# Kernel tuning notes

Measured on AMD Instinct MI355X. Metric: run time of the kernel, lower is better.

The kernel has to match this reference:

```python
import jax, jax.numpy as jnp
import numpy as np
import math

D = 512; NA = 128; NC = 256; NB = 128; BATCH = 4; H = 8
EA, EC, EB = 4, 6, 4
KA, KC, KB = 2, 1, 2
F = 4 * D  # expert_ff_mult * embed_dim
N_TOTAL = NA + NC + NB


def setup_inputs() -> dict:
    key = jax.random.key(0)
    ks = jax.random.split(key, 16)
    s = 0.02
    def nrm(k, shape, scale=s):
        return jax.random.normal(k, shape, dtype=jnp.float32) * scale
    return {
        'tokens_A': jax.random.normal(ks[0], (BATCH, NA, D), dtype=jnp.float32),
        'tokens_B': jax.random.normal(ks[1], (BATCH, NB, D), dtype=jnp.float32),
        'tokens_C': jax.random.normal(ks[2], (BATCH, NC, D), dtype=jnp.float32),
        'ln1_g': jnp.ones((3, D), jnp.float32), 'ln1_b': jnp.zeros((3, D), jnp.float32),
        'ln2_g': jnp.ones((3, D), jnp.float32), 'ln2_b': jnp.zeros((3, D), jnp.float32),
        'Wqkv': nrm(ks[3], (3 * D, D)), 'bqkv': jnp.zeros((3 * D,), jnp.float32),
        'Wo': nrm(ks[4], (D, D)), 'bo': jnp.zeros((D,), jnp.float32),
        'Wr_A': nrm(ks[5], (D, EA)), 'br_A': jnp.zeros((EA,), jnp.float32),
        'W1_A': nrm(ks[6], (EA, D, F)), 'b1_A': jnp.zeros((EA, F), jnp.float32),
        'W2_A': nrm(ks[7], (EA, F, D)), 'b2_A': jnp.zeros((EA, D), jnp.float32),
        'Wr_C': nrm(ks[8], (D, EC)), 'br_C': jnp.zeros((EC,), jnp.float32),
        'W1_C': nrm(ks[9], (EC, D, F)), 'b1_C': jnp.zeros((EC, F), jnp.float32),
        'W2_C': nrm(ks[10], (EC, F, D)), 'b2_C': jnp.zeros((EC, D), jnp.float32),
        'Wr_B': nrm(ks[11], (D, EB)), 'br_B': jnp.zeros((EB,), jnp.float32),
        'W1_B': nrm(ks[12], (EB, D, F)), 'b1_B': jnp.zeros((EB, F), jnp.float32),
        'W2_B': nrm(ks[13], (EB, F, D)), 'b2_B': jnp.zeros((EB, D), jnp.float32),
    }


def _ln(x, g, b, eps=1e-5):
    m = jnp.mean(x, axis=-1, keepdims=True)
    v = jnp.var(x, axis=-1, keepdims=True)
    return (x - m) * jax.lax.rsqrt(v + eps) * g + b


def _directed_mask_bias():
    # segments: 0=A, 1=C, 2=B in [A|C|B] order; query may attend upstream groups only
    seg = jnp.concatenate([jnp.zeros(NA), jnp.ones(NC), 2.0 * jnp.ones(NB)])
    allowed = seg[None, :] <= seg[:, None]  # (N, N)
    return jnp.where(allowed, 0.0, -1e9).astype(jnp.float32)


def _mha(x, Wqkv, bqkv, Wo, bo, mask_bias):
    B, N, _ = x.shape
    qkv = x @ Wqkv.T + bqkv  # (B, N, 3D)
    q, k, v = jnp.split(qkv, 3, axis=-1)
    hd = D // H
    def heads(t):
        return t.reshape(B, N, H, hd).transpose(0, 2, 1, 3)  # (B, H, N, hd)
    q, k, v = heads(q), heads(k), heads(v)
    scores = jnp.einsum('bhqd,bhkd->bhqk', q, k) / math.sqrt(hd) + mask_bias[None, None]
    attn = jax.nn.softmax(scores, axis=-1)
    o = jnp.einsum('bhqk,bhkd->bhqd', attn, v).transpose(0, 2, 1, 3).reshape(B, N, D)
    return o @ Wo.T + bo


def _moe(x, Wr, br, W1, b1, W2, b2, k):
    # top-k routed expert FFN: softmax gates -> top-k renormalized -> dense combine
    probs = jax.nn.softmax(x @ Wr + br, axis=-1)  # (B, N, E)
    vals, idx = jax.lax.top_k(probs, k)
    vals = vals / jnp.sum(vals, axis=-1, keepdims=True)
    E = Wr.shape[1]
    gate = jnp.sum(jax.nn.one_hot(idx, E, dtype=x.dtype) * vals[..., None], axis=-2)  # (B, N, E)
    h = jax.nn.gelu(jnp.einsum('bnd,edf->benf', x, W1) + b1[None, :, None, :])
    y = jnp.einsum('benf,efd->bend', h, W2) + b2[None, :, None, :]
    return jnp.einsum('bne,bend->bnd', gate, y)


def reference(tokens_A, tokens_B, tokens_C, ln1_g, ln1_b, ln2_g, ln2_b,
              Wqkv, bqkv, Wo, bo,
              Wr_A, br_A, W1_A, b1_A, W2_A, b2_A,
              Wr_C, br_C, W1_C, b1_C, W2_C, b2_C,
              Wr_B, br_B, W1_B, b1_B, W2_B, b2_B):
    # 1-2. group-local pre-attention LN, concat [A | C | B]
    x = jnp.concatenate([
        _ln(tokens_A, ln1_g[0], ln1_b[0]),
        _ln(tokens_C, ln1_g[1], ln1_b[1]),
        _ln(tokens_B, ln1_g[2], ln1_b[2]),
    ], axis=1)
    # 3-4. shared directed self-attention + per-group residual
    attn = _mha(x, Wqkv, bqkv, Wo, bo, _directed_mask_bias())
    tA = tokens_A + attn[:, :NA]
    tC = tokens_C + attn[:, NA:NA + NC]
    tB = tokens_B + attn[:, NA + NC:]
    # 5. group-local pre-expert LN
    nA = _ln(tA, ln2_g[0], ln2_b[0])
    nC = _ln(tC, ln2_g[1], ln2_b[1])
    nB = _ln(tB, ln2_g[2], ln2_b[2])
    # 6-9. route A and C first, then B; residual add per group
    tA = tA + _moe(nA, Wr_A, br_A, W1_A, b1_A, W2_A, b2_A, KA)
    tC = tC + _moe(nC, Wr_C, br_C, W1_C, b1_C, W2_C, b2_C, KC)
    tB = tB + _moe(nB, Wr_B, br_B, W1_B, b1_B, W2_B, b2_B, KB)
    return jnp.concatenate([tA, tC, tB], axis=1)  # (B, NA+NC+NB, D)
```

## Files before the change

### kernel.cpp

```cpp
#include <hip/hip_runtime.h>
#include <hip/hip_bf16.h>
#include <cstdint>

#define DEV __device__ __forceinline__

using f32x4  = __attribute__((ext_vector_type(4))) float;
using bf16x8 = __attribute__((ext_vector_type(8))) __bf16;

static constexpr int D_    = 512;
static constexpr int ROWS  = 2048;
static constexpr int F_    = 2048;
static constexpr int NEXP  = 14;
static constexpr int NENT  = 3072;

#if defined(__has_builtin)
#if __has_builtin(__builtin_amdgcn_global_load_lds)
#define HAS_GLL 1
#endif
#endif

DEV unsigned short f2bf(float f) {
  unsigned int u = __builtin_bit_cast(unsigned int, f);
  unsigned int r = u + 0x7FFFu + ((u >> 16) & 1u);
  return (unsigned short)(r >> 16);
}
DEV unsigned int pack2(float a, float b) {
  return (unsigned int)f2bf(a) | ((unsigned int)f2bf(b) << 16);
}
DEV float gelu_tanh(float x) {
  float x3 = x * x * x;
  return 0.5f * x * (1.0f + tanhf(0.7978845608028654f * (x + 0.044715f * x3)));
}
DEV int prefix_base(const int* cnt, int e) {
  int base = 0;
  for (int i = 0; i < e; ++i) base += cnt[i];
  return base;
}

struct Shared128 { unsigned short As[128][72]; unsigned short Bs[64][72]; };

DEV void gemm128(const unsigned short* arow, const float* B, int ldb, int bcol0, int K,
                 f32x4 (&acc)[2][4], Shared128& sh)
{
  const int tid = threadIdx.x;
  const int lane = tid & 63, w = tid >> 6;
  const int ai = tid >> 1, ah = tid & 1;
  const int bj = tid >> 2, bq = tid & 3;
  for (int k0 = 0; k0 < K; k0 += 64) {
    __syncthreads();
    {
      const uint4* src = reinterpret_cast<const uint4*>(arow + k0 + ah * 32);
      uint4 v0 = src[0], v1 = src[1], v2 = src[2], v3 = src[3];
      uint4* dst = reinterpret_cast<uint4*>(&sh.As[ai][ah * 32]);
      dst[0] = v0; dst[1] = v1; dst[2] = v2; dst[3] = v3;
    }
    {
      const float4* src = reinterpret_cast<const float4*>(B + (size_t)(bcol0 + bj) * ldb + k0 + bq * 16);
      unsigned int pk[8];
      #pragma unroll
      for (int u = 0; u < 4; ++u) {
        float4 f = src[u];
        pk[u * 2]     = pack2(f.x, f.y);
        pk[u * 2 + 1] = pack2(f.z, f.w);
      }
      uint4* dst = reinterpret_cast<uint4*>(&sh.Bs[bj][bq * 16]);
      dst[0] = make_uint4(pk[0], pk[1], pk[2], pk[3]);
      dst[1] = make_uint4(pk[4], pk[5], pk[6], pk[7]);
    }
    __syncthreads();
    #pragma unroll
    for (int ks = 0; ks < 2; ++ks) {
      bf16x8 a[2], b[4];
      #pragma unroll
      for (int mi = 0; mi < 2; ++mi)
        a[mi] = *reinterpret_cast<const bf16x8*>(&sh.As[w * 32 + mi * 16 + (lane & 15)][ks * 32 + (lane >> 4) * 8]);
      #pragma unroll
      for (int ni = 0; ni < 4; ++ni)
        b[ni] = *reinterpret_cast<const bf16x8*>(&sh.Bs[ni * 16 + (lane & 15)][ks * 32 + (lane >> 4) * 8]);
      #pragma unroll
      for (int mi = 0; mi < 2; ++mi)
        #pragma unroll
        for (int ni = 0; ni < 4; ++ni)
          acc[mi][ni] = __builtin_amdgcn_mfma_f32_16x16x32_bf16(a[mi], b[ni], acc[mi][ni], 0, 0, 0);
    }
  }
}

struct __align__(16) SharedMoE { unsigned short As[64][72]; unsigned short Bs[8192]; };

DEV void gemm64x128L(const unsigned short* arow, const unsigned short* Bt,
                     f32x4 (&acc)[8], SharedMoE& sh)
{
  const int tid = threadIdx.x;
  const int lane = tid & 63, w = tid >> 6;
  const int ar = tid >> 2, aq = tid & 3;
  #pragma unroll
  for (int kt = 0; kt < 8; ++kt) {
    __syncthreads();
#ifdef HAS_GLL
    {
      const unsigned short* src = Bt + kt * 8192 + w * 2048 + lane * 8;
      unsigned short* dstBase = &sh.Bs[w * 2048];
      #pragma unroll
      for (int i = 0; i < 4; ++i)
        __builtin_amdgcn_global_load_lds(
            (const __attribute__((address_space(1))) unsigned int*)(src + i * 512),
            (__attribute__((address_space(3))) unsigned int*)(dstBase + i * 512),
            16, 0, 0);
    }
#else
    {
      const uint4* srcB = reinterpret_cast<const uint4*>(Bt + kt * 8192 + tid * 32);
      uint4 b0 = srcB[0], b1 = srcB[1], b2 = srcB[2], b3 = srcB[3];
      uint4* dstB = reinterpret_cast<uint4*>(&sh.Bs[tid * 32]);
      dstB[0] = b0; dstB[1] = b1; dstB[2] = b2; dstB[3] = b3;
    }
#endif
    {
      const uint4* srcA = reinterpret_cast<const uint4*>(arow + kt * 64 + aq * 16);
      uint4 a0 = srcA[0], a1 = srcA[1];
      uint4* dstA = reinterpret_cast<uint4*>(&sh.As[ar][aq * 16]);
      dstA[0] = a0; dstA[1] = a1;
    }
    __syncthreads();
    bf16x8 a0 = *reinterpret_cast<const bf16x8*>(&sh.As[w * 16 + (lane & 15)][0 * 32 + (lane >> 4) * 8]);
    bf16x8 a1 = *reinterpret_cast<const bf16x8*>(&sh.As[w * 16 + (lane & 15)][1 * 32 + (lane >> 4) * 8]);
    #pragma unroll
    for (int ni = 0; ni < 8; ++ni) {
      bf16x8 b0 = *reinterpret_cast<const bf16x8*>(&sh.Bs[(ni * 2 + 0) * 512 + lane * 8]);
      bf16x8 b1 = *reinterpret_cast<const bf16x8*>(&sh.Bs[(ni * 2 + 1) * 512 + lane * 8]);
      acc[ni] = __builtin_amdgcn_mfma_f32_16x16x32_bf16(a0, b0, acc[ni], 0, 0, 0);
      acc[ni] = __builtin_amdgcn_mfma_f32_16x16x32_bf16(a1, b1, acc[ni], 0, 0, 0);
    }
  }
}

__global__ __launch_bounds__(256) void k_ln(
    const float* tA, const float* tC, const float* tB,
    const float* g3, const float* b3, unsigned short* out)
{
  int r = blockIdx.x;
  int b = r >> 9, n = r & 511;
  int grp = n < 128 ? 0 : (n < 384 ? 1 : 2);
  const float* src = grp == 0 ? tA + (size_t)(b * 128 + n) * D_
                   : grp == 1 ? tC + (size_t)(b * 256 + n - 128) * D_
                              : tB + (size_t)(b * 128 + n - 384) * D_;
  int tid = threadIdx.x, lane = tid & 63, w = tid >> 6;
  float2 v = *reinterpret_cast<const float2*>(src + tid * 2);
  float s = v.x + v.y;
  float ss = v.x * v.x + v.y * v.y;
  #pragma unroll
  for (int off = 1; off < 64; off <<= 1) { s += __shfl_xor(s, off); ss += __shfl_xor(ss, off); }
  __shared__ float red[8];
  if (lane == 0) { red[w] = s; red[4 + w] = ss; }
  __syncthreads();
  float S  = red[0] + red[1] + red[2] + red[3];
  float SS = red[4] + red[5] + red[6] + red[7];
  float mean = S * (1.0f / 512.0f);
  float var  = SS * (1.0f / 512.0f) - mean * mean;
  float inv  = rsqrtf(var + 1e-5f);
  const float* gam = g3 + grp * D_;
  const float* bet = b3 + grp * D_;
  int d0 = tid * 2;
  out[(size_t)r * D_ + d0]     = f2bf((v.x - mean) * inv * gam[d0]     + bet[d0]);
  out[(size_t)r * D_ + d0 + 1] = f2bf((v.y - mean) * inv * gam[d0 + 1] + bet[d0 + 1]);
}

__global__ __launch_bounds__(256) void k_qkv_pack(
    const unsigned short* x, const float* Wqkv, const float* bqkv,
    unsigned short* Qg, unsigned short* Kg, unsigned short* Vg,
    const float* w1A, const float* w1C, const float* w1B,
    const float* w2A, const float* w2C, const float* w2B,
    unsigned short* W1P, unsigned short* W2P)
{
  __shared__ __align__(16) char smem[sizeof(Shared128)];
  int bid = blockIdx.x;
  int tid = threadIdx.x;
  if (bid < 384) {
    Shared128& sh = *reinterpret_cast<Shared128*>(smem);
    int bn = bid % 24, bm = (bid / 24) % 4, batch = bid / 96;
    int lane = tid & 63, w = tid >> 6;
    const unsigned short* arow = x + (size_t)(batch * 512 + bm * 128 + (tid >> 1)) * D_;
    f32x4 acc[2][4] = {};
    gemm128(arow, Wqkv, 512, bn * 64, 512, acc, sh);
    #pragma unroll
    for (int mi = 0; mi < 2; ++mi)
    #pragma unroll
    for (int ni = 0; ni < 4; ++ni)
    #pragma unroll
    for (int j = 0; j < 4; ++j) {
      int n = bm * 128 + w * 32 + mi * 16 + ((lane >> 4) << 2) + j;
      int col = bn * 64 + ni * 16 + (lane & 15);
      float val = acc[mi][ni][j] + bqkv[col];
      int part = col >> 9;
      int o = col & 511, h = o >> 6, d = o & 63;
      unsigned short* dst = part == 0 ? Qg : (part == 1 ? Kg : Vg);
      dst[(size_t)((batch * 8 + h) * 512 + n) * 64 + d] = f2bf(val);
    }
  } else {
    int pbid = bid - 384;
    int bx = pbid & 127, z = pbid >> 7;
    const float* src;
    unsigned short* dstbase;
    int ld, ntile, ktile, KT;
    if (z < 14) {
      int e = z;
      src = e < 4 ? w1A + (size_t)e * D_ * F_ : e < 10 ? w1C + (size_t)(e - 4) * D_ * F_ : w1B + (size_t)(e - 10) * D_ * F_;
      dstbase = W1P + (size_t)e * F_ * D_;
      ld = F_; KT = 8;
      ntile = bx >> 3; ktile = bx & 7;
    } else {
      int e = z - 14;
      src = e < 4 ? w2A + (size_t)e * F_ * D_ : e < 10 ? w2C + (size_t)(e - 4) * F_ * D_ : w2B + (size_t)(e - 10) * F_ * D_;
      dstbase = W2P + (size_t)e * D_ * F_;
      ld = D_; KT = 32;
      ntile = bx >> 5; ktile = bx & 31;
    }
    int k0 = ktile * 64, n0 = ntile * 128;
    auto sh = reinterpret_cast<unsigned short (*)[138]>(smem);
    {
      int r = tid >> 2, q = tid & 3;
      const float4* sp = reinterpret_cast<const float4*>(src + (size_t)(k0 + r) * ld + n0 + q * 32);
      unsigned int* shw = reinterpret_cast<unsigned int*>(&sh[r][q * 32]);
      #pragma unroll
      for (int u = 0; u < 8; ++u) {
        float4 v = sp[u];
        shw[u * 2]     = pack2(v.x, v.y);
        shw[u * 2 + 1] = pack2(v.z, v.w);
      }
    }
    __syncthreads();
    size_t tbase = (size_t)(ntile * KT + ktile) * 8192;
    #pragma unroll
    for (int i = 0; i < 4; ++i) {
      int p = tid + 256 * i;
      int f = p >> 6, l = p & 63;
      int ks = f & 1, ni = f >> 1;
      int nl = ni * 16 + (l & 15);
      int kl = ks * 32 + (l >> 4) * 8;
      unsigned short tmp[8];
      #pragma unroll
      for (int j = 0; j < 8; ++j) tmp[j] = sh[kl + j][nl];
      *reinterpret_cast<uint4*>(dstbase + tbase + (size_t)p * 8) = *reinterpret_cast<const uint4*>(tmp);
    }
  }
}

__global__ __launch_bounds__(64) void k_attn(const unsigned short* Qg, const unsigned short* Kg,
                                             const unsigned short* Vg, unsigned short* attn)
{
  __shared__ unsigned short Qs[16][72], Ks[64][72], VT[64][72], Ps[16][72];
  int qt16 = blockIdx.x, h = blockIdx.y, b = blockIdx.z;
  int lane = threadIdx.x;
  const unsigned short* Qb  = Qg + (size_t)((b * 8 + h) * 512) * 64;
  const unsigned short* Kbp = Kg + (size_t)((b * 8 + h) * 512) * 64;
  const unsigned short* Vbp = Vg + (size_t)((b * 8 + h) * 512) * 64;
  int q0 = qt16 * 16;
  {
    int row = lane >> 2, q4 = lane & 3;
    const uint4* src = reinterpret_cast<const uint4*>(Qb + (size_t)(q0 + row) * 64 + q4 * 16);
    uint4* dst = reinterpret_cast<uint4*>(&Qs[row][q4 * 16]);
    dst[0] = src[0]; dst[1] = src[1];
  }
  int nkt = qt16 < 8 ? 2 : (qt16 < 24 ? 6 : 8);
  float mrun[4] = { -1e30f, -1e30f, -1e30f, -1e30f };
  float lrun[4] = {};
  f32x4 o[4] = {};
  for (int kt = 0; kt < nkt; ++kt) {
    #pragma unroll
    for (int it = 0; it < 4; ++it) {
      int row = it * 16 + (lane >> 2), q4 = lane & 3;
      const uint4* ksrc = reinterpret_cast<const uint4*>(Kbp + (size_t)(kt * 64 + row) * 64 + q4 * 16);
      uint4* kdst = reinterpret_cast<uint4*>(&Ks[row][q4 * 16]);
      kdst[0] = ksrc[0]; kdst[1] = ksrc[1];
      union { uint4 u; unsigned short s[8]; } vv0, vv1;
      const uint4* vsrc = reinterpret_cast<const uint4*>(Vbp + (size_t)(kt * 64 + row) * 64 + q4 * 16);
      vv0.u = vsrc[0]; vv1.u = vsrc[1];
      #pragma unroll
      for (int jj = 0; jj < 8; ++jj) {
        VT[q4 * 16 + jj][row]     = vv0.s[jj];
        VT[q4 * 16 + 8 + jj][row] = vv1.s[jj];
      }
    }
    f32x4 s[4] = {};
    #pragma unroll
    for (int ks = 0; ks < 2; ++ks) {
      bf16x8 aq = *reinterpret_cast<const bf16x8*>(&Qs[lane & 15][ks * 32 + (lane >> 4) * 8]);
      #pragma unroll
      for (int cc = 0; cc < 4; ++cc) {
        bf16x8 bk = *reinterpret_cast<const bf16x8*>(&Ks[cc * 16 + (lane & 15)][ks * 32 + (lane >> 4) * 8]);
        s[cc] = __builtin_amdgcn_mfma_f32_16x16x32_bf16(aq, bk, s[cc], 0, 0, 0);
      }
    }
    #pragma unroll
    for (int rr = 0; rr < 4; ++rr) {
      float s0 = s[0][rr] * 0.125f, s1 = s[1][rr] * 0.125f;
      float s2 = s[2][rr] * 0.125f, s3 = s[3][rr] * 0.125f;
      float mx = fmaxf(fmaxf(s0, s1), fmaxf(s2, s3));
      #pragma unroll
      for (int off = 1; off < 16; off <<= 1) mx = fmaxf(mx, __shfl_xor(mx, off));
      float mn = fmaxf(mrun[rr], mx);
      float al = expf(mrun[rr] - mn);
      mrun[rr] = mn;
      float p0 = expf(s0 - mn), p1 = expf(s1 - mn), p2 = expf(s2 - mn), p3 = expf(s3 - mn);
      float ps = p0 + p1 + p2 + p3;
      #pragma unroll
      for (int off = 1; off < 16; off <<= 1) ps += __shfl_xor(ps, off);
      lrun[rr] = lrun[rr] * al + ps;
      #pragma unroll
      for (int n4 = 0; n4 < 4; ++n4) o[n4][rr] *= al;
      int prow = ((lane >> 4) << 2) + rr;
      Ps[prow][0 * 16 + (lane & 15)] = f2bf(p0);
      Ps[prow][1 * 16 + (lane & 15)] = f2bf(p1);
      Ps[prow][2 * 16 + (lane & 15)] = f2bf(p2);
      Ps[prow][3 * 16 + (lane & 15)] = f2bf(p3);
    }
    #pragma unroll
    for (int ks = 0; ks < 2; ++ks) {
      bf16x8 ap = *reinterpret_cast<const bf16x8*>(&Ps[lane & 15][ks * 32 + (lane >> 4) * 8]);
      #pragma unroll
      for (int n4 = 0; n4 < 4; ++n4) {
        bf16x8 bv = *reinterpret_cast<const bf16x8*>(&VT[n4 * 16 + (lane & 15)][ks * 32 + (lane >> 4) * 8]);
        o[n4] = __builtin_amdgcn_mfma_f32_16x16x32_bf16(ap, bv, o[n4], 0, 0, 0);
      }
    }
  }
  #pragma unroll
  for (int n4 = 0; n4 < 4; ++n4)
  #pragma unroll
  for (int rr = 0; rr < 4; ++rr) {
    int qrow = q0 + ((lane >> 4) << 2) + rr;
    int col = h * 64 + n4 * 16 + (lane & 15);
    float val = o[n4][rr] / lrun[rr];
    attn[(size_t)(b * 512 + qrow) * 512 + col] = f2bf(val);
  }
}

__global__ __launch_bounds__(256) void k_wo(const unsigned short* attn, const float* Wo, const float* bo,
                                            const float* tokA, const float* tokC, const float* tokB,
                                            float* out)
{
  __shared__ Shared128 sh;
  int bn = blockIdx.x, bm = blockIdx.y;
  int tid = threadIdx.x, lane = tid & 63, w = tid >> 6;
  const unsigned short* arow = attn + (size_t)(bm * 128 + (tid >> 1)) * D_;
  f32x4 acc[2][4] = {};
  gemm128(arow, Wo, 512, bn * 64, 512, acc, sh);
  #pragma unroll
  for (int mi = 0; mi < 2; ++mi)
  #pragma unroll
  for (int ni = 0; ni < 4; ++ni)
  #pragma unroll
  for (int j = 0; j < 4; ++j) {
    int row = bm * 128 + w * 32 + mi * 16 + ((lane >> 4) << 2) + j;
    int col = bn * 64 + ni * 16 + (lane & 15);
    float val = acc[mi][ni][j] + bo[col];
    int b = row >> 9, n = row & 511;
    float res;
    if (n < 128)      res = tokA[(size_t)(b * 128 + n) * D_ + col];
    else if (n < 384) res = tokC[(size_t)(b * 256 + n - 128) * D_ + col];
    else              res = tokB[(size_t)(b * 128 + n - 384) * D_ + col];
    out[(size_t)row * D_ + col] = res + val;
  }
}

__global__ __launch_bounds__(256) void k_router(const float* t,
    const float* ln2g, const float* ln2b,
    const float* WrA, const float* brA, const float* WrC, const float* brC,
    const float* WrB, const float* brB,
    int* cnt, int* tokexp, float* tokgate, unsigned short* nrm)
{
  int w = threadIdx.x >> 6, lane = threadIdx.x & 63;
  int r = blockIdx.x * 4 + w;
  int n = r & 511;
  int grp = n < 128 ? 0 : (n < 384 ? 1 : 2);
  int E = grp == 1 ? 6 : 4;
  int topk = grp == 1 ? 1 : 2;
  int egbase = grp == 0 ? 0 : (grp == 1 ? 4 : 10);
  const float* Wr = grp == 0 ? WrA : (grp == 1 ? WrC : WrB);
  const float* br = grp == 0 ? brA : (grp == 1 ? brC : brB);
  const float* tr = t + (size_t)r * D_;
  float xv[8];
  float s = 0.0f, ss = 0.0f;
  #pragma unroll
  for (int it = 0; it < 8; ++it) {
    float v = tr[it * 64 + lane];
    xv[it] = v; s += v; ss += v * v;
  }
  #pragma unroll
  for (int off = 1; off < 64; off <<= 1) { s += __shfl_xor(s, off); ss += __shfl_xor(ss, off); }
  float mean = s * (1.0f / 512.0f);
  float var  = ss * (1.0f / 512.0f) - mean * mean;
  float inv  = rsqrtf(var + 1e-5f);
  const float* gam = ln2g + grp * D_;
  const float* bet = ln2b + grp * D_;
  float acc[6] = {};
  #pragma unroll
  for (int it = 0; it < 8; ++it) {
    int d = it * 64 + lane;
    float nv = (xv[it] - mean) * inv * gam[d] + bet[d];
    nrm[(size_t)r * D_ + d] = f2bf(nv);
    #pragma unroll
    for (int e = 0; e < 6; ++e) if (e < E) acc[e] += nv * Wr[d * E + e];
  }
  #pragma unroll
  for (int e = 0; e < 6; ++e)
    #pragma unroll
    for (int off = 1; off < 64; off <<= 1) acc[e] += __shfl_xor(acc[e], off);
  if (lane == 0) {
    float p[6];
    float mx = -1e30f;
    #pragma unroll
    for (int e = 0; e < 6; ++e) if (e < E) { p[e] = acc[e] + br[e]; mx = fmaxf(mx, p[e]); }
    float sum = 0.0f;
    #pragma unroll
    for (int e = 0; e < 6; ++e) if (e < E) { p[e] = expf(p[e] - mx); sum += p[e]; }
    #pragma unroll
    for (int e = 0; e < 6; ++e) if (e < E) p[e] /= sum;
    int i1 = 0; float v1 = p[0];
    #pragma unroll
    for (int e = 1; e < 6; ++e) if (e < E && p[e] > v1) { v1 = p[e]; i1 = e; }
    if (topk == 1) {
      tokexp[r * 2]     = egbase + i1; tokgate[r * 2]     = 1.0f;
      tokexp[r * 2 + 1] = -1;          tokgate[r * 2 + 1] = 0.0f;
      atomicAdd(&cnt[egbase + i1], 1);
    } else {
      int i2 = -1; float v2 = -1e30f;
      #pragma unroll
      for (int e = 0; e < 6; ++e) if (e < E && e != i1 && p[e] > v2) { v2 = p[e]; i2 = e; }
      float tot = v1 + v2;
      tokexp[r * 2]     = egbase + i1; tokgate[r * 2]     = v1 / tot;
      tokexp[r * 2 + 1] = egbase + i2; tokgate[r * 2 + 1] = v2 / tot;
      atomicAdd(&cnt[egbase + i1], 1);
      atomicAdd(&cnt[egbase + i2], 1);
    }
  }
}

__global__ __launch_bounds__(256) void k_scatter(const int* tokexp, const float* tokgate,
                                                 const int* cnt, int* cursor, int* list, float* gate)
{
  int r = blockIdx.x * 256 + threadIdx.x;
  #pragma unroll
  for (int j = 0; j < 2; ++j) {
    int e = tokexp[r * 2 + j];
    if (e >= 0) {
      int base = prefix_base(cnt, e);
      int s = atomicAdd(&cursor[e], 1);
      list[base + s] = r;
      gate[base + s] = tokgate[r * 2 + j];
    }
  }
}

__global__ __launch_bounds__(256) void k_moe1(const unsigned short* nrm, const unsigned short* W1P,
    const float* b1A, const float* b1C, const float* b1B,
    const int* cnt, const int* list, unsigned short* H)
{
  int ft = blockIdx.x, tt = blockIdx.y, e = blockIdx.z;
  int c = cnt[e];
  if (tt * 64 >= c) return;
  __shared__ SharedMoE sh;
  const float* b1 = e < 4 ? b1A + (size_t)e * F_ : e < 10 ? b1C + (size_t)(e - 4) * F_ : b1B + (size_t)(e - 10) * F_;
  const unsigned short* Bt = W1P + (size_t)e * F_ * D_ + (size_t)(ft * 8) * 8192;
  int base = prefix_base(cnt, e);
  int tid = threadIdx.x, lane = tid & 63, w = tid >> 6;
  int ig = tt * 64 + (tid >> 2);
  int tok = list[base + (ig < c ? ig : c - 1)];
  const unsigned short* arow = nrm + (size_t)tok * D_;
  f32x4 acc[8] = {};
  gemm64x128L(arow, Bt, acc, sh);
  #pragma unroll
  for (int ni = 0; ni < 8; ++ni)
  #pragma unroll
  for (int j = 0; j < 4; ++j) {
    int rl = w * 16 + ((lane >> 4) << 2) + j;
    int sg = tt * 64 + rl;
    if (sg < c) {
      int col = ft * 128 + ni * 16 + (lane & 15);
      float val = acc[ni][j] + b1[col];
      H[(size_t)(base + sg) * F_ + col] = f2bf(gelu_tanh(val));
    }
  }
}

__global__ __launch_bounds__(256) void k_moe2(const unsigned short* H, const unsigned short* W2P,
    const float* b2A, const float* b2C, const float* b2B,
    const int* cnt, const int* list, const float* gate, float* out)
{
  int dt = blockIdx.x, tt = blockIdx.y >> 2, kc = blockIdx.y & 3, e = blockIdx.z;
  int c = cnt[e];
  if (tt * 64 >= c) return;
  __shared__ SharedMoE sh;
  const float* b2 = e < 4 ? b2A + (size_t)e * D_ : e < 10 ? b2C + (size_t)(e - 4) * D_ : b2B + (size_t)(e - 10) * D_;
  const unsigned short* Bt = W2P + (size_t)e * D_ * F_ + (size_t)(dt * 32 + kc * 8) * 8192;
  int base = prefix_base(cnt, e);
  int tid = threadIdx.x, lane = tid & 63, w = tid >> 6;
  int ig = tt * 64 + (tid >> 2);
  const unsigned short* arow = H + (size_t)(base + (ig < c ? ig : c - 1)) * F_ + kc * 512;
  f32x4 acc[8] = {};
  gemm64x128L(arow, Bt, acc, sh);
  #pragma unroll
  for (int ni = 0; ni < 8; ++ni)
  #pragma unroll
  for (int j = 0; j < 4; ++j) {
    int rl = w * 16 + ((lane >> 4) << 2) + j;
    int sg = tt * 64 + rl;
    if (sg < c) {
      int col = dt * 128 + ni * 16 + (lane & 15);
      float val = acc[ni][j] + (kc == 0 ? b2[col] : 0.0f);
      int tok = list[base + sg];
      atomicAdd(&out[(size_t)tok * D_ + col], gate[base + sg] * val);
    }
  }
}

extern "C" void kernel_launch(void* const* d_in, const int* in_sizes, int n_in,
                              void* d_out, int out_size, void* d_ws, size_t ws_size,
                              hipStream_t stream)
{
  const float* tokA = (const float*)d_in[0];
  const float* tokB = (const float*)d_in[1];
  const float* tokC = (const float*)d_in[2];
  const float* ln1g = (const float*)d_in[3];
  const float* ln1b = (const float*)d_in[4];
  const float* ln2g = (const float*)d_in[5];
  const float* ln2b = (const float*)d_in[6];
  const float* Wqkv = (const float*)d_in[7];
  const float* bqkv = (const float*)d_in[8];
  const float* Wo   = (const float*)d_in[9];
  const float* bo   = (const float*)d_in[10];
  const float* WrA  = (const float*)d_in[11];
  const float* brA  = (const float*)d_in[12];
  const float* W1A  = (const float*)d_in[13];
  const float* b1A  = (const float*)d_in[14];
  const float* W2A  = (const float*)d_in[15];
  const float* b2A  = (const float*)d_in[16];
  const float* WrC  = (const float*)d_in[17];
  const float* brC  = (const float*)d_in[18];
  const float* W1C  = (const float*)d_in[19];
  const float* b1C  = (const float*)d_in[20];
  const float* W2C  = (const float*)d_in[21];
  const float* b2C  = (const float*)d_in[22];
  const float* WrB  = (const float*)d_in[23];
  const float* brB  = (const float*)d_in[24];
  const float* W1B  = (const float*)d_in[25];
  const float* b1B  = (const float*)d_in[26];
  const float* W2B  = (const float*)d_in[27];
  const float* b2B  = (const float*)d_in[28];
  float* out = (float*)d_out;

  char* ws = (char*)d_ws;
  const size_t MB = 1024 * 1024;
  const size_t WSTRIDE = (size_t)NEXP * F_ * D_ * 2;
  unsigned short* xb   = (unsigned short*)(ws);
  unsigned short* nrm  = xb;
  unsigned short* Qg   = (unsigned short*)(ws + 2 * MB);
  unsigned short* Kg   = (unsigned short*)(ws + 4 * MB);
  unsigned short* Vg   = (unsigned short*)(ws + 6 * MB);
  unsigned short* attn = (unsigned short*)(ws + 8 * MB);
  unsigned short* W1P  = (unsigned short*)(ws + 16 * MB);
  unsigned short* W2P  = (unsigned short*)(ws + 16 * MB + WSTRIDE);
  unsigned short* H    = (unsigned short*)(ws + 16 * MB + 2 * WSTRIDE);
  char* small = ws + 16 * MB + 2 * WSTRIDE + (size_t)NENT * F_ * 2;
  int*   cnt     = (int*)(small);
  int*   cursor  = (int*)(small + 64);
  int*   tokexp  = (int*)(small + 256);
  float* tokgate = (float*)(small + 256 + ROWS * 2 * 4);
  int*   list    = (int*)(small + 256 + ROWS * 4 * 4);
  float* gate    = (float*)(small + 256 + ROWS * 4 * 4 + NENT * 4);

  hipMemsetAsync(cnt, 0, 128, stream);
  k_ln<<<ROWS, 256, 0, stream>>>(tokA, tokC, tokB, ln1g, ln1b, xb);
  k_qkv_pack<<<3968, 256, 0, stream>>>(xb, Wqkv, bqkv, Qg, Kg, Vg,
                                       W1A, W1C, W1B, W2A, W2C, W2B, W1P, W2P);
  k_attn<<<dim3(32, 8, 4), 64, 0, stream>>>(Qg, Kg, Vg, attn);
  k_wo<<<dim3(8, 16), 256, 0, stream>>>(attn, Wo, bo, tokA, tokC, tokB, out);
  k_router<<<512, 256, 0, stream>>>(out, ln2g, ln2b, WrA, brA, WrC, brC, WrB, brB,
                                    cnt, tokexp, tokgate, nrm);
  k_scatter<<<8, 256, 0, stream>>>(tokexp, tokgate, cnt, cursor, list, gate);
  k_moe1<<<dim3(16, 16, 14), 256, 0, stream>>>(nrm, W1P, b1A, b1C, b1B, cnt, list, H);
  k_moe2<<<dim3(4, 64, 14), 256, 0, stream>>>(H, W2P, b2A, b2C, b2B, cnt, list, gate, out);
}
```

Before: 211.3 us.

## Spread MoE weight packing across QKV, Wo and router kernels

Packing the MoE expert weights from fp32 to tiled bf16 used to run as 3584 extra blocks inside the QKV kernel. It is now split into three chunks of 1200, 1200 and 1184 blocks, appended to the QKV, Wo and router launches. The aim is to fill the otherwise underoccupied Wo (128 blocks) and router launches with independent bandwidth work and shorten the QKV launch. The risk is that pack blocks compete with the critical-path blocks for bandwidth and CU slots, and the router kernel now carries a larger shared memory allocation.

```diff
diff --git a/kernel.cpp b/kernel.cpp
--- a/kernel.cpp
+++ b/kernel.cpp
@@ -132,6 +132,56 @@
       acc[ni] = __builtin_amdgcn_mfma_f32_16x16x32_bf16(a0, b0, acc[ni], 0, 0, 0);
       acc[ni] = __builtin_amdgcn_mfma_f32_16x16x32_bf16(a1, b1, acc[ni], 0, 0, 0);
     }
+  }
+}
+
+DEV void pack_body(int pbid, int tid, unsigned short (*sh)[138],
+                   const float* w1A, const float* w1C, const float* w1B,
+                   const float* w2A, const float* w2C, const float* w2B,
+                   unsigned short* W1P, unsigned short* W2P)
+{
+  int bx = pbid & 127, z = pbid >> 7;
+  const float* src;
+  unsigned short* dstbase;
+  int ld, ntile, ktile, KT;
+  if (z < 14) {
+    int e = z;
+    src = e < 4 ? w1A + (size_t)e * D_ * F_ : e < 10 ? w1C + (size_t)(e - 4) * D_ * F_ : w1B + (size_t)(e - 10) * D_ * F_;
+    dstbase = W1P + (size_t)e * F_ * D_;
+    ld = F_; KT = 8;
+    ntile = bx >> 3; ktile = bx & 7;
+  } else {
+    int e = z - 14;
+    src = e < 4 ? w2A + (size_t)e * F_ * D_ : e < 10 ? w2C + (size_t)(e - 4) * F_ * D_ : w2B + (size_t)(e - 10) * F_ * D_;
+    dstbase = W2P + (size_t)e * D_ * F_;
+    ld = D_; KT = 32;
+    ntile = bx >> 5; ktile = bx & 31;
+  }
+  int k0 = ktile * 64, n0 = ntile * 128;
+  {
+    int r = tid >> 2, q = tid & 3;
+    const float4* sp = reinterpret_cast<const float4*>(src + (size_t)(k0 + r) * ld + n0 + q * 32);
+    unsigned int* shw = reinterpret_cast<unsigned int*>(&sh[r][q * 32]);
+    #pragma unroll
+    for (int u = 0; u < 8; ++u) {
+      float4 v = sp[u];
+      shw[u * 2]     = pack2(v.x, v.y);
+      shw[u * 2 + 1] = pack2(v.z, v.w);
+    }
+  }
+  __syncthreads();
+  size_t tbase = (size_t)(ntile * KT + ktile) * 8192;
+  #pragma unroll
+  for (int i = 0; i < 4; ++i) {
+    int p = tid + 256 * i;
+    int f = p >> 6, l = p & 63;
+    int ks = f & 1, ni = f >> 1;
+    int nl = ni * 16 + (l & 15);
+    int kl = ks * 32 + (l >> 4) * 8;
+    unsigned short tmp[8];
+    #pragma unroll
+    for (int j = 0; j < 8; ++j) tmp[j] = sh[kl + j][nl];
+    *reinterpret_cast<uint4*>(dstbase + tbase + (size_t)p * 8) = *reinterpret_cast<const uint4*>(tmp);
   }
 }
 
@@ -198,51 +248,8 @@
       dst[(size_t)((batch * 8 + h) * 512 + n) * 64 + d] = f2bf(val);
     }
   } else {
-    int pbid = bid - 384;
-    int bx = pbid & 127, z = pbid >> 7;
-    const float* src;
-    unsigned short* dstbase;
-    int ld, ntile, ktile, KT;
-    if (z < 14) {
-      int e = z;
-      src = e < 4 ? w1A + (size_t)e * D_ * F_ : e < 10 ? w1C + (size_t)(e - 4) * D_ * F_ : w1B + (size_t)(e - 10) * D_ * F_;
-      dstbase = W1P + (size_t)e * F_ * D_;
-      ld = F_; KT = 8;
-      ntile = bx >> 3; ktile = bx & 7;
-    } else {
-      int e = z - 14;
-      src = e < 4 ? w2A + (size_t)e * F_ * D_ : e < 10 ? w2C + (size_t)(e - 4) * F_ * D_ : w2B + (size_t)(e - 10) * F_ * D_;
-      dstbase = W2P + (size_t)e * D_ * F_;
-      ld = D_; KT = 32;
-      ntile = bx >> 5; ktile = bx & 31;
-    }
-    int k0 = ktile * 64, n0 = ntile * 128;
-    auto sh = reinterpret_cast<unsigned short (*)[138]>(smem);
-    {
-      int r = tid >> 2, q = tid & 3;
-      const float4* sp = reinterpret_cast<const float4*>(src + (size_t)(k0 + r) * ld + n0 + q * 32);
-      unsigned int* shw = reinterpret_cast<unsigned int*>(&sh[r][q * 32]);
-      #pragma unroll
-      for (int u = 0; u < 8; ++u) {
-        float4 v = sp[u];
-        shw[u * 2]     = pack2(v.x, v.y);
-        shw[u * 2 + 1] = pack2(v.z, v.w);
-      }
-    }
-    __syncthreads();
-    size_t tbase = (size_t)(ntile * KT + ktile) * 8192;
-    #pragma unroll
-    for (int i = 0; i < 4; ++i) {
-      int p = tid + 256 * i;
-      int f = p >> 6, l = p & 63;
-      int ks = f & 1, ni = f >> 1;
-      int nl = ni * 16 + (l & 15);
-      int kl = ks * 32 + (l >> 4) * 8;
-      unsigned short tmp[8];
-      #pragma unroll
-      for (int j = 0; j < 8; ++j) tmp[j] = sh[kl + j][nl];
-      *reinterpret_cast<uint4*>(dstbase + tbase + (size_t)p * 8) = *reinterpret_cast<const uint4*>(tmp);
-    }
+    pack_body(bid - 384, tid, reinterpret_cast<unsigned short (*)[138]>(smem),
+              w1A, w1C, w1B, w2A, w2C, w2B, W1P, W2P);
   }
 }
 
@@ -336,42 +343,63 @@
   }
 }
 
-__global__ __launch_bounds__(256) void k_wo(const unsigned short* attn, const float* Wo, const float* bo,
-                                            const float* tokA, const float* tokC, const float* tokB,
-                                            float* out)
-{
-  __shared__ Shared128 sh;
-  int bn = blockIdx.x, bm = blockIdx.y;
-  int tid = threadIdx.x, lane = tid & 63, w = tid >> 6;
-  const unsigned short* arow = attn + (size_t)(bm * 128 + (tid >> 1)) * D_;
-  f32x4 acc[2][4] = {};
-  gemm128(arow, Wo, 512, bn * 64, 512, acc, sh);
-  #pragma unroll
-  for (int mi = 0; mi < 2; ++mi)
-  #pragma unroll
-  for (int ni = 0; ni < 4; ++ni)
-  #pragma unroll
-  for (int j = 0; j < 4; ++j) {
-    int row = bm * 128 + w * 32 + mi * 16 + ((lane >> 4) << 2) + j;
-    int col = bn * 64 + ni * 16 + (lane & 15);
-    float val = acc[mi][ni][j] + bo[col];
-    int b = row >> 9, n = row & 511;
-    float res;
-    if (n < 128)      res = tokA[(size_t)(b * 128 + n) * D_ + col];
-    else if (n < 384) res = tokC[(size_t)(b * 256 + n - 128) * D_ + col];
-    else              res = tokB[(size_t)(b * 128 + n - 384) * D_ + col];
-    out[(size_t)row * D_ + col] = res + val;
-  }
-}
-
-__global__ __launch_bounds__(256) void k_router(const float* t,
+__global__ __launch_bounds__(256) void k_wo_pack(
+    const unsigned short* attn, const float* Wo, const float* bo,
+    const float* tokA, const float* tokC, const float* tokB, float* out,
+    const float* w1A, const float* w1C, const float* w1B,
+    const float* w2A, const float* w2C, const float* w2B,
+    unsigned short* W1P, unsigned short* W2P)
+{
+  __shared__ __align__(16) char smem[sizeof(Shared128)];
+  int bid = blockIdx.x;
+  int tid = threadIdx.x;
+  if (bid < 128) {
+    Shared128& sh = *reinterpret_cast<Shared128*>(smem);
+    int bn = bid & 7, bm = bid >> 3;
+    int lane = tid & 63, w = tid >> 6;
+    const unsigned short* arow = attn + (size_t)(bm * 128 + (tid >> 1)) * D_;
+    f32x4 acc[2][4] = {};
+    gemm128(arow, Wo, 512, bn * 64, 512, acc, sh);
+    #pragma unroll
+    for (int mi = 0; mi < 2; ++mi)
+    #pragma unroll
+    for (int ni = 0; ni < 4; ++ni)
+    #pragma unroll
+    for (int j = 0; j < 4; ++j) {
+      int row = bm * 128 + w * 32 + mi * 16 + ((lane >> 4) << 2) + j;
+      int col = bn * 64 + ni * 16 + (lane & 15);
+      float val = acc[mi][ni][j] + bo[col];
+      int b = row >> 9, n = row & 511;
+      float res;
+      if (n < 128)      res = tokA[(size_t)(b * 128 + n) * D_ + col];
+      else if (n < 384) res = tokC[(size_t)(b * 256 + n - 128) * D_ + col];
+      else              res = tokB[(size_t)(b * 128 + n - 384) * D_ + col];
+      out[(size_t)row * D_ + col] = res + val;
+    }
+  } else {
+    pack_body(1200 + bid - 128, tid, reinterpret_cast<unsigned short (*)[138]>(smem),
+              w1A, w1C, w1B, w2A, w2C, w2B, W1P, W2P);
+  }
+}
+
+__global__ __launch_bounds__(256) void k_router_pack(const float* t,
     const float* ln2g, const float* ln2b,
     const float* WrA, const float* brA, const float* WrC, const float* brC,
     const float* WrB, const float* brB,
-    int* cnt, int* tokexp, float* tokgate, unsigned short* nrm)
-{
+    int* cnt, int* tokexp, float* tokgate, unsigned short* nrm,
+    const float* w1A, const float* w1C, const float* w1B,
+    const float* w2A, const float* w2C, const float* w2B,
+    unsigned short* W1P, unsigned short* W2P)
+{
+  __shared__ __align__(16) char smem[64 * 138 * 2];
+  int bid = blockIdx.x;
+  if (bid >= 512) {
+    pack_body(2400 + bid - 512, threadIdx.x, reinterpret_cast<unsigned short (*)[138]>(smem),
+              w1A, w1C, w1B, w2A, w2C, w2B, W1P, W2P);
+    return;
+  }
   int w = threadIdx.x >> 6, lane = threadIdx.x & 63;
-  int r = blockIdx.x * 4 + w;
+  int r = bid * 4 + w;
   int n = r & 511;
   int grp = n < 128 ? 0 : (n < 384 ? 1 : 2);
   int E = grp == 1 ? 6 : 4;
@@ -572,12 +600,14 @@
 
   hipMemsetAsync(cnt, 0, 128, stream);
   k_ln<<<ROWS, 256, 0, stream>>>(tokA, tokC, tokB, ln1g, ln1b, xb);
-  k_qkv_pack<<<3968, 256, 0, stream>>>(xb, Wqkv, bqkv, Qg, Kg, Vg,
-                                       W1A, W1C, W1B, W2A, W2C, W2B, W1P, W2P);
+  k_qkv_pack<<<384 + 1200, 256, 0, stream>>>(xb, Wqkv, bqkv, Qg, Kg, Vg,
+                                             W1A, W1C, W1B, W2A, W2C, W2B, W1P, W2P);
   k_attn<<<dim3(32, 8, 4), 64, 0, stream>>>(Qg, Kg, Vg, attn);
-  k_wo<<<dim3(8, 16), 256, 0, stream>>>(attn, Wo, bo, tokA, tokC, tokB, out);
-  k_router<<<512, 256, 0, stream>>>(out, ln2g, ln2b, WrA, brA, WrC, brC, WrB, brB,
-                                    cnt, tokexp, tokgate, nrm);
+  k_wo_pack<<<128 + 1200, 256, 0, stream>>>(attn, Wo, bo, tokA, tokC, tokB, out,
+                                            W1A, W1C, W1B, W2A, W2C, W2B, W1P, W2P);
+  k_router_pack<<<512 + 1184, 256, 0, stream>>>(out, ln2g, ln2b, WrA, brA, WrC, brC, WrB, brB,
+                                                cnt, tokexp, tokgate, nrm,
+                                                W1A, W1C, W1B, W2A, W2C, W2B, W1P, W2P);
   k_scatter<<<8, 256, 0, stream>>>(tokexp, tokgate, cnt, cursor, list, gate);
   k_moe1<<<dim3(16, 16, 14), 256, 0, stream>>>(nrm, W1P, b1A, b1C, b1B, cnt, list, H);
   k_moe2<<<dim3(4, 64, 14), 256, 0, stream>>>(H, W2P, b2A, b2C, b2B, cnt, list, gate, out);
```

New measurement: 207.0 us (median of 2 runs). -2.0%, faster.
